# Optimization experiments

Hardware: AMD Instinct MI355X
Metric: run time of the kernel (lower is better)

The kernel has to match this reference:

```python
import jax, jax.numpy as jnp
import numpy as np

B, T, C, H, L, V = 4, 1024, 1024, 16, 6, 32000
D = C // H
STD = 0.02


def setup_inputs() -> dict:
    key = jax.random.key(0)
    ks = jax.random.split(key, 12)
    return {
        "idx": jax.random.randint(ks[0], (B, T), 0, V),
        "tok_emb": jax.random.normal(ks[1], (V, C), jnp.float32) * STD,
        "pos_emb": jax.random.normal(ks[2], (T, C), jnp.float32) * STD,
        "qkv_w": jax.random.normal(ks[3], (L, C, 3 * C), jnp.float32) * STD,
        "attn_out_w": jax.random.normal(ks[4], (L, C, C), jnp.float32) * STD,
        "attn_out_b": jnp.zeros((L, C), jnp.float32),
        "fc1_w": jax.random.normal(ks[5], (L, C, 4 * C), jnp.float32) * STD,
        "fc1_b": jnp.zeros((L, 4 * C), jnp.float32),
        "fc2_w": jax.random.normal(ks[6], (L, 4 * C, C), jnp.float32) * STD,
        "fc2_b": jnp.zeros((L, C), jnp.float32),
        "ln1_w": jnp.ones((L, C), jnp.float32),
        "ln1_b": jnp.zeros((L, C), jnp.float32),
        "ln2_w": jnp.ones((L, C), jnp.float32),
        "ln2_b": jnp.zeros((L, C), jnp.float32),
        "lnf_w": jnp.ones((C,), jnp.float32),
        "lnf_b": jnp.zeros((C,), jnp.float32),
        "head_w": jax.random.normal(ks[7], (C, V), jnp.float32) * STD,
    }


def layernorm(x, w, b, eps=1e-5):
    mu = jnp.mean(x, axis=-1, keepdims=True)
    var = jnp.var(x, axis=-1, keepdims=True)
    return (x - mu) * jax.lax.rsqrt(var + eps) * w + b


def attention(x, qkv_w, out_w, out_b, causal_mask):
    # x: (B,T,C)
    qkv = jnp.einsum("btc,cf->btf", x, qkv_w)  # (B,T,3C)
    q, k, v = jnp.split(qkv, 3, axis=-1)
    q = q.reshape(B, T, H, D).transpose(0, 2, 1, 3)  # (B,H,T,D)
    k = k.reshape(B, T, H, D).transpose(0, 2, 1, 3)
    v = v.reshape(B, T, H, D).transpose(0, 2, 1, 3)
    scores = jnp.einsum("bhqd,bhkd->bhqk", q, k) / np.sqrt(D).astype(np.float32)
    scores = jnp.where(causal_mask, scores, -jnp.inf)
    w = jax.nn.softmax(scores, axis=-1)
    out = jnp.einsum("bhqk,bhkd->bhqd", w, v)  # (B,H,T,D)
    out = out.transpose(0, 2, 1, 3).reshape(B, T, C)
    return jnp.einsum("btc,cd->btd", out, out_w) + out_b


def reference(idx, tok_emb, pos_emb, qkv_w, attn_out_w, attn_out_b,
              fc1_w, fc1_b, fc2_w, fc2_b, ln1_w, ln1_b, ln2_w, ln2_b,
              lnf_w, lnf_b, head_w):
    causal_mask = jnp.tril(jnp.ones((T, T), dtype=bool))[None, None]  # (1,1,T,T)
    x = tok_emb[idx] + pos_emb[jnp.arange(T)][None]  # (B,T,C)
    for l in range(L):
        h = layernorm(x, ln1_w[l], ln1_b[l])
        x = x + attention(h, qkv_w[l], attn_out_w[l], attn_out_b[l], causal_mask)
        h = layernorm(x, ln2_w[l], ln2_b[l])
        h = jax.nn.relu(jnp.einsum("btc,cf->btf", h, fc1_w[l]) + fc1_b[l])
        x = x + jnp.einsum("btf,fc->btc", h, fc2_w[l]) + fc2_b[l]
    x = layernorm(x, lnf_w, lnf_b)
    logits = jnp.einsum("btc,cv->btv", x, head_w)  # (B,T,V)
    return logits
```

## Files before the change

kernel.cpp:

```cpp
#include <hip/hip_runtime.h>
#include <cstdint>
#include <cstddef>

typedef __bf16 bf16_t;
typedef __bf16 bf16x8 __attribute__((ext_vector_type(8)));
typedef float f32x4 __attribute__((ext_vector_type(4)));
typedef int i32x4 __attribute__((ext_vector_type(4)));

#define B_ 4
#define T_ 1024
#define C_ 1024
#define H_ 16
#define L_ 6
#define V_ 32000
#define M_ (B_ * T_)

__global__ __launch_bounds__(256) void k_embed(const int* __restrict__ idx,
                                               const float* __restrict__ tok,
                                               const float* __restrict__ pos,
                                               float* __restrict__ x) {
  int row = blockIdx.x;
  int t = row & (T_ - 1);
  int id = idx[row];
  int c = threadIdx.x * 4;
  f32x4 a = *(const f32x4*)(tok + (size_t)id * C_ + c);
  f32x4 p = *(const f32x4*)(pos + (size_t)t * C_ + c);
  *(f32x4*)(x + (size_t)row * C_ + c) = a + p;
}

__global__ __launch_bounds__(256) void k_ln(const float* __restrict__ x,
                                            const float* __restrict__ w,
                                            const float* __restrict__ b,
                                            bf16_t* __restrict__ out) {
  __shared__ float red[8];
  int row = blockIdx.x;
  int tid = threadIdx.x;
  const float* xr = x + (size_t)row * C_;
  f32x4 v = *(const f32x4*)(xr + tid * 4);
  float s = v[0] + v[1] + v[2] + v[3];
  float q = v[0] * v[0] + v[1] * v[1] + v[2] * v[2] + v[3] * v[3];
#pragma unroll
  for (int off = 32; off; off >>= 1) {
    s += __shfl_xor(s, off);
    q += __shfl_xor(q, off);
  }
  int wid = tid >> 6;
  if ((tid & 63) == 0) { red[wid * 2] = s; red[wid * 2 + 1] = q; }
  __syncthreads();
  s = red[0] + red[2] + red[4] + red[6];
  q = red[1] + red[3] + red[5] + red[7];
  float mu = s * (1.f / C_);
  float var = q * (1.f / C_) - mu * mu;
  float rstd = rsqrtf(var + 1e-5f);
  f32x4 wv = *(const f32x4*)(w + tid * 4);
  f32x4 bv = *(const f32x4*)(b + tid * 4);
  bf16_t* o = out + (size_t)row * C_ + tid * 4;
#pragma unroll
  for (int j = 0; j < 4; j++) o[j] = (bf16_t)((v[j] - mu) * rstd * wv[j] + bv[j]);
}

__global__ __launch_bounds__(256) void k_transpose_bf16(const float* __restrict__ in,
                                                        bf16_t* __restrict__ out,
                                                        int K, int N) {
  __shared__ float tile[32][33];
  int n0 = blockIdx.x * 32, k0 = blockIdx.y * 32;
  int tid = threadIdx.x;
  int cr = tid >> 5, cc = tid & 31;
#pragma unroll
  for (int it = 0; it < 4; it++) {
    int r = it * 8 + cr;
    tile[r][cc] = in[(size_t)(k0 + r) * N + n0 + cc];
  }
  __syncthreads();
#pragma unroll
  for (int it = 0; it < 4; it++) {
    int r = it * 8 + cr;
    out[(size_t)(n0 + r) * K + k0 + cc] = (bf16_t)tile[cc][r];
  }
}

__global__ __launch_bounds__(256) void k_reshape_qk(const bf16_t* __restrict__ qkv,
                                                    bf16_t* __restrict__ qh,
                                                    bf16_t* __restrict__ kh) {
  int g = blockIdx.x * 256 + threadIdx.x;
  int d = g & 63;
  int t = (g >> 6) & (T_ - 1);
  int h = (g >> 16) & (H_ - 1);
  int b = g >> 20;
  size_t src = ((size_t)(b * T_ + t)) * (3 * C_) + h * 64 + d;
  qh[g] = (bf16_t)((float)qkv[src] * 0.125f);
  kh[g] = qkv[src + C_];
}

__global__ __launch_bounds__(256) void k_vtrans(const bf16_t* __restrict__ qkv,
                                                bf16_t* __restrict__ vT) {
  __shared__ bf16_t tile[64][65];
  int bh = blockIdx.x;
  int t0 = blockIdx.y * 64;
  int tid = threadIdx.x;
  int c = tid & 63, rr = tid >> 6;
  int b = bh >> 4, h = bh & (H_ - 1);
  const bf16_t* src = qkv + ((size_t)(b * T_ + t0)) * (3 * C_) + 2 * C_ + h * 64;
#pragma unroll
  for (int it = 0; it < 16; it++) {
    int r = it * 4 + rr;
    tile[r][c] = src[(size_t)r * (3 * C_) + c];
  }
  __syncthreads();
  bf16_t* dst = vT + (size_t)bh * 64 * T_ + t0;
#pragma unroll
  for (int it = 0; it < 16; it++) {
    int dr = it * 4 + rr;
    dst[(size_t)dr * T_ + c] = tile[c][dr];
  }
}

__global__ __launch_bounds__(256) void k_attn(const bf16_t* __restrict__ qh,
                                              const bf16_t* __restrict__ kh,
                                              const bf16_t* __restrict__ vT,
                                              bf16_t* __restrict__ outb) {
  __shared__ bf16_t p_lds[4][16 * 32];
  int tid = threadIdx.x, lane = tid & 63, wid = tid >> 6;
  int bh = blockIdx.x;
  int b = bh >> 4, h = bh & (H_ - 1);
  int qbase = blockIdx.y * 64 + wid * 16;
  const bf16_t* qp = qh + ((size_t)bh * T_ + qbase) * 64;
  const bf16_t* kp = kh + (size_t)bh * T_ * 64;
  const bf16_t* vp = vT + (size_t)bh * 64 * T_;
  int r = lane & 15, g = lane >> 4;

  bf16x8 qf0 = *(const bf16x8*)(qp + r * 64 + g * 8);
  bf16x8 qf1 = *(const bf16x8*)(qp + r * 64 + 32 + g * 8);

  f32x4 o[4];
  float m[4], l[4];
#pragma unroll
  for (int j = 0; j < 4; j++) { m[j] = -1e30f; l[j] = 0.f; o[j] = (f32x4){0.f, 0.f, 0.f, 0.f}; }

  int kv_end = qbase + 16;
  for (int jb = 0; jb < kv_end; jb += 32) {
    f32x4 s0 = (f32x4){0.f, 0.f, 0.f, 0.f};
    f32x4 s1 = (f32x4){0.f, 0.f, 0.f, 0.f};
    const bf16_t* kb0 = kp + (size_t)(jb + r) * 64 + g * 8;
    const bf16_t* kb1 = kb0 + 16 * 64;
    s0 = __builtin_amdgcn_mfma_f32_16x16x32_bf16(qf0, *(const bf16x8*)(kb0), s0, 0, 0, 0);
    s0 = __builtin_amdgcn_mfma_f32_16x16x32_bf16(qf1, *(const bf16x8*)(kb0 + 32), s0, 0, 0, 0);
    s1 = __builtin_amdgcn_mfma_f32_16x16x32_bf16(qf0, *(const bf16x8*)(kb1), s1, 0, 0, 0);
    s1 = __builtin_amdgcn_mfma_f32_16x16x32_bf16(qf1, *(const bf16x8*)(kb1 + 32), s1, 0, 0, 0);

    float p0[4], p1[4], fac[4];
#pragma unroll
    for (int j = 0; j < 4; j++) {
      int rowg = qbase + g * 4 + j;
      float v0 = s0[j], v1 = s1[j];
      if (jb + r > rowg) v0 = -1e30f;
      if (jb + 16 + r > rowg) v1 = -1e30f;
      float t = fmaxf(v0, v1);
      t = fmaxf(t, __shfl_xor(t, 1));
      t = fmaxf(t, __shfl_xor(t, 2));
      t = fmaxf(t, __shfl_xor(t, 4));
      t = fmaxf(t, __shfl_xor(t, 8));
      float nm = fmaxf(m[j], t);
      p0[j] = __expf(v0 - nm);
      p1[j] = __expf(v1 - nm);
      float f = __expf(m[j] - nm);
      float ts = p0[j] + p1[j];
      ts += __shfl_xor(ts, 1);
      ts += __shfl_xor(ts, 2);
      ts += __shfl_xor(ts, 4);
      ts += __shfl_xor(ts, 8);
      l[j] = l[j] * f + ts;
      m[j] = nm;
      fac[j] = f;
    }
    f32x4 fv = (f32x4){fac[0], fac[1], fac[2], fac[3]};
#pragma unroll
    for (int d = 0; d < 4; d++) o[d] *= fv;

    bf16_t* pl = p_lds[wid];
#pragma unroll
    for (int j = 0; j < 4; j++) {
      pl[(g * 4 + j) * 32 + r] = (bf16_t)p0[j];
      pl[(g * 4 + j) * 32 + 16 + r] = (bf16_t)p1[j];
    }
    bf16x8 pa = *(const bf16x8*)(pl + r * 32 + g * 8);
#pragma unroll
    for (int d = 0; d < 4; d++) {
      const bf16_t* vf = vp + (size_t)(d * 16 + r) * T_ + jb + g * 8;
      o[d] = __builtin_amdgcn_mfma_f32_16x16x32_bf16(pa, *(const bf16x8*)(vf), o[d], 0, 0, 0);
    }
  }

#pragma unroll
  for (int d = 0; d < 4; d++) {
#pragma unroll
    for (int j = 0; j < 4; j++) {
      float val = o[d][j] / l[j];
      outb[((size_t)(b * T_ + qbase + g * 4 + j)) * C_ + h * 64 + d * 16 + r] = (bf16_t)val;
    }
  }
}

__device__ __forceinline__ void gld_lds16(const bf16_t* g, bf16_t* l) {
  __builtin_amdgcn_global_load_lds((const __attribute__((address_space(1))) void*)g,
                                   (__attribute__((address_space(3))) void*)l, 16, 0, 0);
}
__device__ __forceinline__ bf16x8 lds_rd128(uint32_t addr) {
  i32x4 d;
  asm volatile("ds_read_b128 %0, %1" : "=v"(d) : "v"(addr));
  return __builtin_bit_cast(bf16x8, d);
}
#define BAR_() __builtin_amdgcn_s_barrier()
#define SCHED0_() __builtin_amdgcn_sched_barrier(0)
#define WLGN_(n)                                                           \
  do {                                                                     \
    asm volatile("s_waitcnt lgkmcnt(" #n ")" ::: "memory");                \
    SCHED0_();                                                             \
  } while (0)

template <int OUTBF, int HASB, int HASRELU, int HASRES>
__global__ __launch_bounds__(256) void k_gemm(const bf16_t* __restrict__ A,
                                              const bf16_t* __restrict__ Bt,
                                              const float* __restrict__ bias,
                                              const float* resid,
                                              void* Cout, int M, int N, int K) {
  __shared__ bf16_t As[2][128 * 32];
  __shared__ bf16_t Bs[2][128 * 32];
  int tid = threadIdx.x;
  int lane = tid & 63, wid = tid >> 6;

  int nwg = (int)(gridDim.x * gridDim.y);
  int bid = (int)(blockIdx.y * gridDim.x + blockIdx.x);
  int xcd = bid & 7, loc = bid >> 3;
  int q8 = nwg >> 3, r8 = nwg & 7;
  int swz = (xcd < r8) ? xcd * (q8 + 1) + loc : r8 * (q8 + 1) + (xcd - r8) * q8 + loc;
  int nY = M >> 7;
  size_t rowBase = (size_t)(swz % nY) * 128;
  size_t colBase = (size_t)(swz / nY) * 128;

  int scolE = (((tid & 3) ^ ((tid >> 2) & 3) ^ ((tid >> 4) & 3)) * 8);
  const bf16_t* gA = A + (rowBase + (tid >> 2)) * (size_t)K + scolE;
  const bf16_t* gB = Bt + (colBase + (tid >> 2)) * (size_t)K + scolE;
  const size_t gStep64 = (size_t)64 * K;

  f32x4 acc[4][4];
#pragma unroll
  for (int i = 0; i < 4; i++)
#pragma unroll
    for (int j = 0; j < 4; j++) acc[i][j] = (f32x4){0.f, 0.f, 0.f, 0.f};

  int NK = K >> 5;
  {
    bf16_t* la = &As[0][0] + wid * 512;
    bf16_t* lb = &Bs[0][0] + wid * 512;
    gld_lds16(gA, la);            gld_lds16(gA + gStep64, la + 2048);
    gld_lds16(gB, lb);            gld_lds16(gB + gStep64, lb + 2048);
  }

  int wr = (wid >> 1) * 64, wc = (wid & 1) * 64;
  int r15 = lane & 15, g4 = lane >> 4;
  uint32_t roff = (uint32_t)((g4 * 8) ^ (((r15 & 3) ^ ((r15 >> 2) & 3)) << 3));

  for (int kt = 0; kt < NK; kt++) {
    int buf = kt & 1;
    __syncthreads();
    if (kt + 1 < NK) {
      const bf16_t* ga = gA + (size_t)(kt + 1) * 32;
      const bf16_t* gb = gB + (size_t)(kt + 1) * 32;
      bf16_t* la = &As[buf ^ 1][0] + wid * 512;
      bf16_t* lb = &Bs[buf ^ 1][0] + wid * 512;
      gld_lds16(ga, la);          gld_lds16(ga + gStep64, la + 2048);
      gld_lds16(gb, lb);          gld_lds16(gb + gStep64, lb + 2048);
    }
    const bf16_t* asb = &As[buf][0];
    const bf16_t* bsb = &Bs[buf][0];
    bf16x8 af[4], bfr[4];
#pragma unroll
    for (int i = 0; i < 4; i++)
      af[i] = *(const bf16x8*)(asb + (wr + r15 + i * 16) * 32 + roff);
#pragma unroll
    for (int i = 0; i < 4; i++)
      bfr[i] = *(const bf16x8*)(bsb + (wc + r15 + i * 16) * 32 + roff);
#pragma unroll
    for (int i = 0; i < 4; i++)
#pragma unroll
      for (int j = 0; j < 4; j++)
        acc[i][j] = __builtin_amdgcn_mfma_f32_16x16x32_bf16(af[i], bfr[j], acc[i][j], 0, 0, 0);
  }

#pragma unroll
  for (int i = 0; i < 4; i++) {
    size_t row0 = rowBase + wr + i * 16 + g4 * 4;
#pragma unroll
    for (int j = 0; j < 4; j++) {
      size_t col = colBase + wc + j * 16 + r15;
      float bi = HASB ? bias[col] : 0.f;
#pragma unroll
      for (int q = 0; q < 4; q++) {
        size_t row = row0 + q;
        float v = acc[i][j][q] + bi;
        if (HASRELU) v = fmaxf(v, 0.f);
        if (HASRES) v += resid[row * (size_t)N + col];
        if (OUTBF)
          ((bf16_t*)Cout)[row * (size_t)N + col] = (bf16_t)v;
        else
          ((float*)Cout)[row * (size_t)N + col] = v;
      }
    }
  }
}

#define STAGE_(q, tk, bufv)                                                           \
  do {                                                                                \
    const bf16_t* _ga = A + (size_t)(rowBase + (q)*64 + srow) * (size_t)K +           \
                        (size_t)(tk)*64 + scol;                                       \
    const bf16_t* _gb = Bt + (size_t)(colBase + (q)*64 + srow) * (size_t)K +          \
                        (size_t)(tk)*64 + scol;                                       \
    gld_lds16(_ga, AsF + (bufv)*16384 + (q)*4096 + w * 512);                          \
    gld_lds16(_gb, BsF + (bufv)*16384 + (q)*4096 + w * 512);                          \
  } while (0)

#define RDS_(aset, bset, kk, bufv)                                                    \
  do {                                                                                \
    uint32_t _off = (kk) ? offK1 : offK0;                                             \
    uint32_t _ab = aRd + (uint32_t)(bufv)*32768u + _off;                              \
    uint32_t _bb = bRd + (uint32_t)(bufv)*32768u + _off;                              \
    _Pragma("unroll") for (int _m = 0; _m < 8; _m++)                                  \
        aset[_m] = lds_rd128(_ab + _m * 2048);                                        \
    _Pragma("unroll") for (int _n = 0; _n < 4; _n++)                                  \
        bset[_n] = lds_rd128(_bb + _n * 2048);                                        \
  } while (0)

#define MFH_(aset, bset)                                                              \
  do {                                                                                \
    __builtin_amdgcn_s_setprio(1);                                                    \
    _Pragma("unroll") for (int _m = 0; _m < 8; _m++)                                  \
        _Pragma("unroll") for (int _n = 0; _n < 4; _n++)                              \
            acc[_m][_n] = __builtin_amdgcn_mfma_f32_16x16x32_bf16(                    \
                aset[_m], bset[_n], acc[_m][_n], 0, 0, 0);                            \
    __builtin_amdgcn_s_setprio(0);                                                    \
  } while (0)

template <int OUTBF, int HASB, int HASRELU, int HASRES>
__global__ __launch_bounds__(512, 2) void k_gemm256(const bf16_t* __restrict__ A,
                                                    const bf16_t* __restrict__ Bt,
                                                    const float* __restrict__ bias,
                                                    const float* resid,
                                                    void* Cout, int M, int N, int K) {
  __shared__ bf16_t As[2][256][64];
  __shared__ bf16_t Bs[2][256][64];
  bf16_t* AsF = &As[0][0][0];
  bf16_t* BsF = &Bs[0][0][0];
  const uint32_t asb = (uint32_t)(uintptr_t)AsF;
  const uint32_t bsb = (uint32_t)(uintptr_t)BsF;

  int tid = threadIdx.x, lane = tid & 63, w = tid >> 6;
  int wr = w >> 2, wc = w & 3;
  int r15 = lane & 15, g4 = lane >> 4;

  int nwg = (int)gridDim.x;
  int bid = (int)blockIdx.x;
  int xcd = bid & 7, loc = bid >> 3;
  int q8 = nwg >> 3, r8 = nwg & 7;
  int swz = (xcd < r8) ? xcd * (q8 + 1) + loc : r8 * (q8 + 1) + (xcd - r8) * q8 + loc;
  int nY = M >> 8;
  int by = swz % nY, bx = swz / nY;
  int rowBase = by * 256, colBase = bx * 256;

  int srow = w * 8 + (lane >> 3);
  int scol = ((lane & 7) ^ (lane >> 3)) * 8;

  uint32_t xm = (uint32_t)((r15 & 7) << 4);
  uint32_t offK0 = ((uint32_t)(g4 * 16)) ^ xm;
  uint32_t offK1 = ((uint32_t)(g4 * 16 + 64)) ^ xm;
  uint32_t aRd = asb + (uint32_t)((wr * 128 + r15) * 128);
  uint32_t bRd = bsb + (uint32_t)((wc * 64 + r15) * 128);

  f32x4 acc[8][4];
#pragma unroll
  for (int i = 0; i < 8; i++)
#pragma unroll
    for (int j = 0; j < 4; j++) acc[i][j] = (f32x4){0.f, 0.f, 0.f, 0.f};

  bf16x8 a0[8], a1[8], b0[4], b1[4];

#pragma unroll
  for (int q = 0; q < 4; q++) STAGE_(q, 0, 0);
  asm volatile("s_waitcnt vmcnt(0)" ::: "memory");
  BAR_();

  int NT = K >> 6;
  for (int kt = 0; kt < NT; ++kt) {
    int buf = kt & 1;
    bool pf = (kt + 1 < NT);
    if (pf) {
#pragma unroll
      for (int q = 0; q < 4; q++) STAGE_(q, kt + 1, buf ^ 1);
    }
    RDS_(a0, b0, 0, buf);
    RDS_(a1, b1, 1, buf);
    WLGN_(12);
    MFH_(a0, b0);
    WLGN_(0);
    MFH_(a1, b1);
    asm volatile("s_waitcnt vmcnt(0)" ::: "memory");
    BAR_();
  }

#pragma unroll
  for (int m = 0; m < 8; m++) {
    size_t row0 = (size_t)rowBase + wr * 128 + m * 16 + g4 * 4;
#pragma unroll
    for (int n = 0; n < 4; n++) {
      size_t col = (size_t)colBase + wc * 64 + n * 16 + r15;
      float bi = HASB ? bias[col] : 0.f;
#pragma unroll
      for (int qq = 0; qq < 4; qq++) {
        size_t row = row0 + qq;
        float v = acc[m][n][qq] + bi;
        if (HASRELU) v = fmaxf(v, 0.f);
        if (HASRES) v += resid[row * (size_t)N + col];
        if (OUTBF)
          ((bf16_t*)Cout)[row * (size_t)N + col] = (bf16_t)v;
        else
          ((float*)Cout)[row * (size_t)N + col] = v;
      }
    }
  }
}

extern "C" void kernel_launch(void* const* d_in, const int* in_sizes, int n_in,
                              void* d_out, int out_size, void* d_ws, size_t ws_size,
                              hipStream_t stream) {
  (void)in_sizes; (void)n_in; (void)out_size; (void)ws_size;
  const int* idx = (const int*)d_in[0];
  const float* tok_emb = (const float*)d_in[1];
  const float* pos_emb = (const float*)d_in[2];
  const float* qkv_w = (const float*)d_in[3];
  const float* attn_out_w = (const float*)d_in[4];
  const float* attn_out_b = (const float*)d_in[5];
  const float* fc1_w = (const float*)d_in[6];
  const float* fc1_b = (const float*)d_in[7];
  const float* fc2_w = (const float*)d_in[8];
  const float* fc2_b = (const float*)d_in[9];
  const float* ln1_w = (const float*)d_in[10];
  const float* ln1_b = (const float*)d_in[11];
  const float* ln2_w = (const float*)d_in[12];
  const float* ln2_b = (const float*)d_in[13];
  const float* lnf_w = (const float*)d_in[14];
  const float* lnf_b = (const float*)d_in[15];
  const float* head_w = (const float*)d_in[16];
  float* out = (float*)d_out;

  char* wsp = (char*)d_ws;
  auto alloc = [&](size_t bytes) {
    char* p = wsp;
    wsp += (bytes + 255) & ~(size_t)255;
    return p;
  };
  float* x      = (float*)alloc((size_t)M_ * C_ * 4);
  bf16_t* hbuf  = (bf16_t*)alloc((size_t)M_ * C_ * 2);
  bf16_t* qkvb  = (bf16_t*)alloc((size_t)M_ * 3 * C_ * 2);
  bf16_t* qhb   = (bf16_t*)alloc((size_t)M_ * C_ * 2);
  bf16_t* khb   = (bf16_t*)alloc((size_t)M_ * C_ * 2);
  bf16_t* vTb   = (bf16_t*)alloc((size_t)M_ * C_ * 2);
  bf16_t* attnb = (bf16_t*)alloc((size_t)M_ * C_ * 2);
  bf16_t* midb  = (bf16_t*)alloc((size_t)M_ * 4 * C_ * 2);
  bf16_t* qkvwT = (bf16_t*)alloc((size_t)3 * C_ * C_ * 2);
  bf16_t* owT   = (bf16_t*)alloc((size_t)C_ * C_ * 2);
  bf16_t* fc1wT = (bf16_t*)alloc((size_t)4 * C_ * C_ * 2);
  bf16_t* fc2wT = (bf16_t*)alloc((size_t)4 * C_ * C_ * 2);
  bf16_t* headwT= (bf16_t*)alloc((size_t)C_ * V_ * 2);

  k_embed<<<M_, 256, 0, stream>>>(idx, tok_emb, pos_emb, x);
  k_transpose_bf16<<<dim3(V_ / 32, C_ / 32), 256, 0, stream>>>(head_w, headwT, C_, V_);

  for (int l = 0; l < L_; l++) {
    k_transpose_bf16<<<dim3(3 * C_ / 32, C_ / 32), 256, 0, stream>>>(
        qkv_w + (size_t)l * C_ * 3 * C_, qkvwT, C_, 3 * C_);
    k_transpose_bf16<<<dim3(C_ / 32, C_ / 32), 256, 0, stream>>>(
        attn_out_w + (size_t)l * C_ * C_, owT, C_, C_);
    k_transpose_bf16<<<dim3(4 * C_ / 32, C_ / 32), 256, 0, stream>>>(
        fc1_w + (size_t)l * C_ * 4 * C_, fc1wT, C_, 4 * C_);
    k_transpose_bf16<<<dim3(C_ / 32, 4 * C_ / 32), 256, 0, stream>>>(
        fc2_w + (size_t)l * 4 * C_ * C_, fc2wT, 4 * C_, C_);

    k_ln<<<M_, 256, 0, stream>>>(x, ln1_w + l * C_, ln1_b + l * C_, hbuf);
    k_gemm256<1, 0, 0, 0><<<dim3((3 * C_ / 256) * (M_ / 256)), 512, 0, stream>>>(
        hbuf, qkvwT, nullptr, nullptr, qkvb, M_, 3 * C_, C_);
    k_reshape_qk<<<(M_ * C_) / 256, 256, 0, stream>>>(qkvb, qhb, khb);
    k_vtrans<<<dim3(B_ * H_, T_ / 64), 256, 0, stream>>>(qkvb, vTb);
    k_attn<<<dim3(B_ * H_, T_ / 64), 256, 0, stream>>>(qhb, khb, vTb, attnb);
    k_gemm<0, 1, 0, 1><<<dim3(C_ / 128, M_ / 128), 256, 0, stream>>>(
        attnb, owT, attn_out_b + l * C_, x, x, M_, C_, C_);

    k_ln<<<M_, 256, 0, stream>>>(x, ln2_w + l * C_, ln2_b + l * C_, hbuf);
    k_gemm256<1, 1, 1, 0><<<dim3((4 * C_ / 256) * (M_ / 256)), 512, 0, stream>>>(
        hbuf, fc1wT, fc1_b + (size_t)l * 4 * C_, nullptr, midb, M_, 4 * C_, C_);
    k_gemm<0, 1, 0, 1><<<dim3(C_ / 128, M_ / 128), 256, 0, stream>>>(
        midb, fc2wT, fc2_b + l * C_, x, x, M_, C_, 4 * C_);
  }

  k_ln<<<M_, 256, 0, stream>>>(x, lnf_w, lnf_b, hbuf);
  k_gemm256<0, 0, 0, 0><<<dim3((V_ / 256) * (M_ / 256)), 512, 0, stream>>>(
      hbuf, headwT, nullptr, nullptr, out, M_, V_, C_);
}
```

Baseline: 2.248 ms.

## Rework 128x128 GEMM to BK=64 with split LDS reads, and use it for QKV/FC1

The 128x128 GEMM kernel now uses a 64-wide K tile with a new XOR swizzle and explicit ds_read_b128 reads split into two k-halves. The first half's MFMAs can start while the second half's reads are still in flight, and setprio is raised around MFMA issue. Launch bounds now request two workgroups per CU. The QKV and FC1 projections switch from the 256x256 512-thread kernel to this 128x128 kernel, which gives more workgroups and better occupancy at the cost of less data reuse per tile.

Result: faster. 2.109 ms (-6.2%).

```diff
diff --git a/kernel.cpp b/kernel.cpp
--- a/kernel.cpp
+++ b/kernel.cpp
@@ -219,15 +219,21 @@
   } while (0)
 
 template <int OUTBF, int HASB, int HASRELU, int HASRES>
-__global__ __launch_bounds__(256) void k_gemm(const bf16_t* __restrict__ A,
-                                              const bf16_t* __restrict__ Bt,
-                                              const float* __restrict__ bias,
-                                              const float* resid,
-                                              void* Cout, int M, int N, int K) {
-  __shared__ bf16_t As[2][128 * 32];
-  __shared__ bf16_t Bs[2][128 * 32];
-  int tid = threadIdx.x;
-  int lane = tid & 63, wid = tid >> 6;
+__global__ __launch_bounds__(256, 2) void k_gemm(const bf16_t* __restrict__ A,
+                                                 const bf16_t* __restrict__ Bt,
+                                                 const float* __restrict__ bias,
+                                                 const float* resid,
+                                                 void* Cout, int M, int N, int K) {
+  __shared__ bf16_t As[2][128][64];
+  __shared__ bf16_t Bs[2][128][64];
+  bf16_t* AsF = &As[0][0][0];
+  bf16_t* BsF = &Bs[0][0][0];
+  const uint32_t asb = (uint32_t)(uintptr_t)AsF;
+  const uint32_t bsb = (uint32_t)(uintptr_t)BsF;
+
+  int tid = threadIdx.x, lane = tid & 63, w = tid >> 6;
+  int wr = w >> 1, wc = w & 1;
+  int r15 = lane & 15, g4 = lane >> 4;
 
   int nwg = (int)(gridDim.x * gridDim.y);
   int bid = (int)(blockIdx.y * gridDim.x + blockIdx.x);
@@ -235,13 +241,18 @@
   int q8 = nwg >> 3, r8 = nwg & 7;
   int swz = (xcd < r8) ? xcd * (q8 + 1) + loc : r8 * (q8 + 1) + (xcd - r8) * q8 + loc;
   int nY = M >> 7;
-  size_t rowBase = (size_t)(swz % nY) * 128;
-  size_t colBase = (size_t)(swz / nY) * 128;
-
-  int scolE = (((tid & 3) ^ ((tid >> 2) & 3) ^ ((tid >> 4) & 3)) * 8);
-  const bf16_t* gA = A + (rowBase + (tid >> 2)) * (size_t)K + scolE;
-  const bf16_t* gB = Bt + (colBase + (tid >> 2)) * (size_t)K + scolE;
-  const size_t gStep64 = (size_t)64 * K;
+  int by = swz % nY, bx = swz / nY;
+  size_t rowBase = (size_t)by * 128;
+  size_t colBase = (size_t)bx * 128;
+
+  int srowL = (lane >> 3);
+  int scol = ((lane & 7) ^ srowL) * 8;
+
+  uint32_t xm = (uint32_t)((r15 & 7) << 4);
+  uint32_t offK0 = ((uint32_t)(g4 * 16)) ^ xm;
+  uint32_t offK1 = ((uint32_t)(g4 * 16 + 64)) ^ xm;
+  uint32_t aRd = asb + (uint32_t)((wr * 64 + r15) * 128);
+  uint32_t bRd = bsb + (uint32_t)((wc * 64 + r15) * 128);
 
   f32x4 acc[4][4];
 #pragma unroll
@@ -249,51 +260,65 @@
 #pragma unroll
     for (int j = 0; j < 4; j++) acc[i][j] = (f32x4){0.f, 0.f, 0.f, 0.f};
 
-  int NK = K >> 5;
-  {
-    bf16_t* la = &As[0][0] + wid * 512;
-    bf16_t* lb = &Bs[0][0] + wid * 512;
-    gld_lds16(gA, la);            gld_lds16(gA + gStep64, la + 2048);
-    gld_lds16(gB, lb);            gld_lds16(gB + gStep64, lb + 2048);
-  }
-
-  int wr = (wid >> 1) * 64, wc = (wid & 1) * 64;
-  int r15 = lane & 15, g4 = lane >> 4;
-  uint32_t roff = (uint32_t)((g4 * 8) ^ (((r15 & 3) ^ ((r15 >> 2) & 3)) << 3));
-
-  for (int kt = 0; kt < NK; kt++) {
+  bf16x8 a0[4], a1[4], b0[4], b1[4];
+
+#define KSTAGE_(tk, bufv)                                                            \
+  do {                                                                               \
+    _Pragma("unroll") for (int _q = 0; _q < 4; _q++) {                               \
+      int _row = _q * 32 + w * 8 + srowL;                                            \
+      const bf16_t* _ga = A + (rowBase + _row) * (size_t)K + (size_t)(tk)*64 + scol; \
+      const bf16_t* _gb = Bt + (colBase + _row) * (size_t)K + (size_t)(tk)*64 + scol;\
+      gld_lds16(_ga, AsF + (bufv)*8192 + _q * 2048 + w * 512);                       \
+      gld_lds16(_gb, BsF + (bufv)*8192 + _q * 2048 + w * 512);                       \
+    }                                                                                \
+  } while (0)
+
+#define KRDS_(aset, bset, kk, bufv)                                                  \
+  do {                                                                               \
+    uint32_t _off = (kk) ? offK1 : offK0;                                            \
+    uint32_t _ab = aRd + (uint32_t)(bufv)*16384u + _off;                             \
+    uint32_t _bb = bRd + (uint32_t)(bufv)*16384u + _off;                             \
+    _Pragma("unroll") for (int _m = 0; _m < 4; _m++)                                 \
+        aset[_m] = lds_rd128(_ab + _m * 2048);                                       \
+    _Pragma("unroll") for (int _n = 0; _n < 4; _n++)                                 \
+        bset[_n] = lds_rd128(_bb + _n * 2048);                                       \
+  } while (0)
+
+#define KMFH_(aset, bset)                                                            \
+  do {                                                                               \
+    __builtin_amdgcn_s_setprio(1);                                                   \
+    _Pragma("unroll") for (int _m = 0; _m < 4; _m++)                                 \
+        _Pragma("unroll") for (int _n = 0; _n < 4; _n++)                             \
+            acc[_m][_n] = __builtin_amdgcn_mfma_f32_16x16x32_bf16(                   \
+                aset[_m], bset[_n], acc[_m][_n], 0, 0, 0);                           \
+    __builtin_amdgcn_s_setprio(0);                                                   \
+  } while (0)
+
+  KSTAGE_(0, 0);
+  asm volatile("s_waitcnt vmcnt(0)" ::: "memory");
+  BAR_();
+
+  int NT = K >> 6;
+  for (int kt = 0; kt < NT; ++kt) {
     int buf = kt & 1;
-    __syncthreads();
-    if (kt + 1 < NK) {
-      const bf16_t* ga = gA + (size_t)(kt + 1) * 32;
-      const bf16_t* gb = gB + (size_t)(kt + 1) * 32;
-      bf16_t* la = &As[buf ^ 1][0] + wid * 512;
-      bf16_t* lb = &Bs[buf ^ 1][0] + wid * 512;
-      gld_lds16(ga, la);          gld_lds16(ga + gStep64, la + 2048);
-      gld_lds16(gb, lb);          gld_lds16(gb + gStep64, lb + 2048);
-    }
-    const bf16_t* asb = &As[buf][0];
-    const bf16_t* bsb = &Bs[buf][0];
-    bf16x8 af[4], bfr[4];
-#pragma unroll
-    for (int i = 0; i < 4; i++)
-      af[i] = *(const bf16x8*)(asb + (wr + r15 + i * 16) * 32 + roff);
-#pragma unroll
-    for (int i = 0; i < 4; i++)
-      bfr[i] = *(const bf16x8*)(bsb + (wc + r15 + i * 16) * 32 + roff);
-#pragma unroll
-    for (int i = 0; i < 4; i++)
-#pragma unroll
-      for (int j = 0; j < 4; j++)
-        acc[i][j] = __builtin_amdgcn_mfma_f32_16x16x32_bf16(af[i], bfr[j], acc[i][j], 0, 0, 0);
+    bool pf = (kt + 1 < NT);
+    if (pf) KSTAGE_(kt + 1, buf ^ 1);
+    KRDS_(a0, b0, 0, buf);
+    KRDS_(a1, b1, 1, buf);
+    WLGN_(8);
+    KMFH_(a0, b0);
+    WLGN_(0);
+    KMFH_(a1, b1);
+    asm volatile("s_waitcnt vmcnt(0)" ::: "memory");
+    BAR_();
   }
 
 #pragma unroll
   for (int i = 0; i < 4; i++) {
-    size_t row0 = rowBase + wr + i * 16 + g4 * 4;
+    size_t row0 = rowBase + wr * 64 + i * 16 + g4 * 4;
 #pragma unroll
     for (int j = 0; j < 4; j++) {
-      size_t col = colBase + wc + j * 16 + r15;
+      size_t col = colBase + wc * 64 + j * 16 + r15;
       float bi = HASB ? bias[col] : 0.f;
 #pragma unroll
       for (int q = 0; q < 4; q++) {
@@ -308,6 +333,9 @@
       }
     }
   }
+#undef KSTAGE_
+#undef KRDS_
+#undef KMFH_
 }
 
 #define STAGE_(q, tk, bufv)                                                           \
@@ -486,7 +514,7 @@
         fc2_w + (size_t)l * 4 * C_ * C_, fc2wT, 4 * C_, C_);
 
     k_ln<<<M_, 256, 0, stream>>>(x, ln1_w + l * C_, ln1_b + l * C_, hbuf);
-    k_gemm256<1, 0, 0, 0><<<dim3((3 * C_ / 256) * (M_ / 256)), 512, 0, stream>>>(
+    k_gemm<1, 0, 0, 0><<<dim3(3 * C_ / 128, M_ / 128), 256, 0, stream>>>(
         hbuf, qkvwT, nullptr, nullptr, qkvb, M_, 3 * C_, C_);
     k_reshape_qk<<<(M_ * C_) / 256, 256, 0, stream>>>(qkvb, qhb, khb);
     k_vtrans<<<dim3(B_ * H_, T_ / 64), 256, 0, stream>>>(qkvb, vTb);
@@ -495,7 +523,7 @@
         attnb, owT, attn_out_b + l * C_, x, x, M_, C_, C_);
 
     k_ln<<<M_, 256, 0, stream>>>(x, ln2_w + l * C_, ln2_b + l * C_, hbuf);
-    k_gemm256<1, 1, 1, 0><<<dim3((4 * C_ / 256) * (M_ / 256)), 512, 0, stream>>>(
+    k_gemm<1, 1, 1, 0><<<dim3(4 * C_ / 128, M_ / 128), 256, 0, stream>>>(
         hbuf, fc1wT, fc1_b + (size_t)l * 4 * C_, nullptr, midb, M_, 4 * C_, C_);
     k_gemm<0, 1, 0, 1><<<dim3(C_ / 128, M_ / 128), 256, 0, stream>>>(
         midb, fc2wT, fc2_b + l * C_, x, x, M_, C_, 4 * C_);
```
